# Kernel optimization log

Hardware: AMD Instinct MI355X
Metric: run time of the kernel (lower is better)

Reference implementation:

```python
import jax, jax.numpy as jnp
import numpy as np

K = 3  # n_neighbors


def setup_inputs() -> dict:
    key = jax.random.key(0)
    k1, k2, k3 = jax.random.split(key, 3)
    N, D, C, B = 400000, 27, 11, 512  # train size, 3*N_PEAKS_MAX, classes, query batch
    train_features = jax.random.normal(k1, (N, D), dtype=jnp.float32)
    label_idx = jax.random.randint(k2, (N,), 0, C)
    train_labels = jax.nn.one_hot(label_idx, C, dtype=jnp.float32)
    query = jax.random.normal(k3, (B, D), dtype=jnp.float32)
    return {"query": query, "train_features": train_features, "train_labels": train_labels}


def _divide_no_nan(x, y):
    # tf.math.divide_no_nan: 0 where denominator is 0
    y_safe = jnp.where(y != 0, y, 1.0)
    return jnp.where(y != 0, x / y_safe, 0.0)


def reference(query, train_features, train_labels):
    # scale = per-feature max abs over training set (computed in __init__)
    scale = jnp.max(jnp.abs(train_features), axis=0)            # [D]
    train_s = _divide_no_nan(train_features, scale)             # [N,D]
    q_s = _divide_no_nan(query, scale)                          # [B,D]

    xn = jnp.sum(train_s * train_s, axis=1)                     # [N]
    qn = jnp.sum(q_s * q_s, axis=1)                             # [B]
    d2 = qn[:, None] - 2.0 * jnp.einsum('bd,nd->bn', q_s, train_s) + xn[None, :]
    dist = jnp.sqrt(jnp.maximum(d2, 0.0))                       # [B,N]

    neg_kd, idx = jax.lax.top_k(-dist, K)                       # k smallest distances
    kd = -neg_kd                                                # [B,K]

    lab = train_labels[idx]                                     # [B,K,C]
    # inverse-distance weighted vote (safe against zero distances)
    kd_safe = jnp.where(kd == 0.0, 1.0, kd)
    votes = jnp.sum(lab / kd_safe[:, :, None], axis=1)          # [B,C]
    vote_res = jax.nn.one_hot(jnp.argmax(votes, axis=1), train_labels.shape[1], dtype=jnp.float32)

    # exact-match branch: if the nearest distance is 0, return its label directly
    zero_hit = (jnp.min(kd, axis=1) == 0.0)[:, None]            # [B,1]
    result = jnp.where(zero_hit, lab[:, 0, :], vote_res)        # [B,C]
    return kd, result
```

## Files before the change

kernel.cpp:

```cpp
#include <hip/hip_runtime.h>
#include <math.h>

typedef _Float16 h8 __attribute__((ext_vector_type(8)));
typedef float    f4v __attribute__((ext_vector_type(4)));

#define N_TRAIN 400000
#define DIMS    27
#define BQ      512
#define NCLS    11
#define KNN     3
#define NB      500
#define TPB     512
#define PTS_BLK 800
#define PTS_SUP 160
#define NSUP    5
#define NPT     10
#define RAWF    4320
#define TILE_B  2048
#define NC      (NB * KNN)
#define SB      512
#define RPB     784
#define SROWS   128
#define P2T     512

__global__ __launch_bounds__(256) void k_scale(const float* __restrict__ train,
                                               unsigned* __restrict__ scale_u) {
    __shared__ float st[SROWS * DIMS];
    __shared__ float sp[243];
    int tid = threadIdx.x;
    int r0 = blockIdx.x * RPB;
    int r1 = min(r0 + RPB, N_TRAIN);
    int c  = tid % DIMS;
    int rr = tid / DIMS;
    float m = 0.f;
    for (int base = r0; base < r1; base += SROWS) {
        int cnt = min(SROWS, r1 - base);
        int tot4 = (cnt * DIMS) >> 2;
        const uint4* src4 = (const uint4*)(train + (size_t)base * DIMS);
        uint4* st4 = (uint4*)st;
        for (int i = tid; i < tot4; i += 256) st4[i] = src4[i];
        __syncthreads();
        if (tid < 243) {
            for (int r = rr; r < cnt; r += 9)
                m = fmaxf(m, fabsf(st[r * DIMS + c]));
        }
        __syncthreads();
    }
    if (tid < 243) sp[tid] = m;
    __syncthreads();
    if (tid < DIMS) {
        float v = 0.f;
#pragma unroll
        for (int g = 0; g < 9; ++g) v = fmaxf(v, sp[g * DIMS + tid]);
        atomicMax(&scale_u[tid], __float_as_uint(v));
    }
}

__global__ __launch_bounds__(TPB) void k_qprep(const float* __restrict__ query,
                                               const unsigned* __restrict__ scale_u,
                                               _Float16* __restrict__ Qhi,
                                               _Float16* __restrict__ Qlo) {
    int q = threadIdx.x;
    if (q >= BQ) return;
    const float* r = query + (size_t)q * DIMS;
#pragma unroll
    for (int d = 0; d < 32; ++d) {
        _Float16 hi = (_Float16)0.f, lo = (_Float16)0.f;
        if (d < DIMS) {
            float sc = __uint_as_float(scale_u[d]);
            float inv = (sc != 0.f) ? 1.f / sc : 0.f;
            float xs = r[d] * inv;
            hi = (_Float16)xs;
            lo = (_Float16)(xs - (float)hi);
        } else if (d == 27) {
            hi = (_Float16)1.f;
        }
        Qhi[q * 32 + d] = hi;
        Qlo[q * 32 + d] = lo;
    }
}

#define TOP2(A, GI, B0, B1, I0, I1) do { \
    bool c0_ = (A) > (B0); \
    bool c1_ = (A) > (B1); \
    B1 = c0_ ? (B0) : (c1_ ? (A) : (B1)); \
    I1 = c0_ ? (I0) : (c1_ ? (GI) : (I1)); \
    B0 = c0_ ? (A) : (B0); \
    I0 = c0_ ? (GI) : (I0); \
} while (0)

__device__ __forceinline__ void insert3(float d, int i, float* bd, int* bi) {
    if (d < bd[2] || (d == bd[2] && i < bi[2])) {
        if (d < bd[1] || (d == bd[1] && i < bi[1])) {
            bd[2] = bd[1]; bi[2] = bi[1];
            if (d < bd[0] || (d == bd[0] && i < bi[0])) {
                bd[1] = bd[0]; bi[1] = bi[0];
                bd[0] = d; bi[0] = i;
            } else { bd[1] = d; bi[1] = i; }
        } else { bd[2] = d; bi[2] = i; }
    }
}

__device__ __forceinline__ void stage16(const float* g, float* l) {
    __builtin_amdgcn_global_load_lds((const __attribute__((address_space(1))) void*)g,
                                     (__attribute__((address_space(3))) void*)l, 16, 0, 0);
}

__global__ __attribute__((amdgpu_flat_work_group_size(TPB, TPB)))
__attribute__((amdgpu_waves_per_eu(4, 4)))
void k_pass1(const float* __restrict__ train,
             const unsigned* __restrict__ scale_u,
             const _Float16* __restrict__ Qhi,
             const _Float16* __restrict__ Qlo,
             float* __restrict__ cand_d,
             int* __restrict__ cand_i) {
    __shared__ float s_inv[32];
    __shared__ __align__(16) float raw[2][RAWF];
    __shared__ __align__(16) unsigned char conv[NPT * TILE_B];

    int tid = threadIdx.x;
    if (tid < 32) {
        float sc = __uint_as_float(scale_u[tid]);
        s_inv[tid] = (sc != 0.f) ? 1.f / sc : 0.f;
    }
    int lane = tid & 63, w = tid >> 6;
    int l15 = lane & 15, quad = lane >> 4;

    h8 bhi[4], blo[4];
#pragma unroll
    for (int j = 0; j < 4; ++j) {
        int qt = w * 4 + j;
        size_t e = (size_t)(qt * 16 + l15) * 32 + quad * 8;
        bhi[j] = *(const h8*)(Qhi + e);
        blo[j] = *(const h8*)(Qlo + e);
    }

    float b0[4], b1[4];
    int   i0[4], i1[4];
#pragma unroll
    for (int j = 0; j < 4; ++j) { b0[j] = -3.4e38f; b1[j] = -3.4e38f; i0[j] = 0x7fffffff; i1[j] = 0x7fffffff; }

    int p0 = blockIdx.x * PTS_BLK;
    const float* gsup = train + (size_t)p0 * DIMS;

    {
        const float* gp = gsup; float* lp = raw[0];
        stage16(gp + tid * 4, lp + tid * 4);
        stage16(gp + 2048 + tid * 4, lp + 2048 + tid * 4);
        if (tid < 56) stage16(gp + 4096 + tid * 4, lp + 4096 + tid * 4);
    }

    for (int s = 0; s < NSUP; ++s) {
        __syncthreads();

        const float* rw = raw[s & 1];
#pragma unroll
        for (int pass = 0; pass < 2; ++pass) {
            int task = tid + pass * TPB;
            if (task < PTS_SUP * 4) {
                int p = task >> 2, gq = task & 3;
                float x[8]; float part = 0.f;
#pragma unroll
                for (int i = 0; i < 8; ++i) {
                    int d = gq * 8 + i;
                    int dc = d < DIMS ? d : (DIMS - 1);
                    float v = rw[p * DIMS + dc] * s_inv[d];
                    x[i] = v;
                    part = fmaf(v, v, part);
                }
                part += __shfl_xor(part, 1, 64);
                part += __shfl_xor(part, 2, 64);
                h8 hv, lv;
#pragma unroll
                for (int i = 0; i < 8; ++i) {
                    _Float16 h = (_Float16)x[i];
                    hv[i] = h;
                    lv[i] = (_Float16)(x[i] - (float)h);
                }
                if (gq == 3) {
                    float tt = -0.5f * part;
                    _Float16 th = (_Float16)tt;
                    hv[3] = th;
                    lv[3] = (_Float16)(tt - (float)th);
                }
                unsigned char* dstb = conv + (p >> 4) * TILE_B + gq * 256 + (p & 15) * 16;
                *(h8*)dstb = hv;
                *(h8*)(dstb + 1024) = lv;
            }
        }
        __syncthreads();

        if (s + 1 < NSUP) {
            const float* gp = gsup + (size_t)(s + 1) * RAWF;
            float* lp = raw[(s + 1) & 1];
            stage16(gp + tid * 4, lp + tid * 4);
            stage16(gp + 2048 + tid * 4, lp + 2048 + tid * 4);
            if (tid < 56) stage16(gp + 4096 + tid * 4, lp + 4096 + tid * 4);
        }

        for (int t = 0; t < NPT; ++t) {
            const unsigned char* basep = conv + t * TILE_B;
            h8 ahi = *(const h8*)(basep + lane * 16);
            h8 alo = *(const h8*)(basep + 1024 + lane * 16);
            int gbase = p0 + (s * NPT + t) * 16 + quad * 4;
#pragma unroll
            for (int j = 0; j < 4; ++j) {
                f4v acc = {0.f, 0.f, 0.f, 0.f};
                acc = __builtin_amdgcn_mfma_f32_16x16x32_f16(alo, bhi[j], acc, 0, 0, 0);
                acc = __builtin_amdgcn_mfma_f32_16x16x32_f16(ahi, blo[j], acc, 0, 0, 0);
                acc = __builtin_amdgcn_mfma_f32_16x16x32_f16(ahi, bhi[j], acc, 0, 0, 0);
#pragma unroll
                for (int r = 0; r < 4; ++r)
                    TOP2(acc[r], gbase + r, b0[j], b1[j], i0[j], i1[j]);
            }
        }
    }

    int g = blockIdx.x;
#pragma unroll
    for (int j = 0; j < 4; ++j) {
        float kk[3] = {-b0[j], -b1[j], 3.4e38f};
        int   ii[3] = {i0[j], i1[j], 0x7fffffff};
#pragma unroll
        for (int step = 16; step <= 32; step <<= 1) {
            float od[3]; int oi[3];
#pragma unroll
            for (int k = 0; k < 3; ++k) {
                od[k] = __shfl_xor(kk[k], step, 64);
                oi[k] = __shfl_xor(ii[k], step, 64);
            }
#pragma unroll
            for (int k = 0; k < 3; ++k) insert3(od[k], oi[k], kk, ii);
        }
        if (quad == 0) {
            int qq = (w * 4 + j) * 16 + l15;
            size_t off = (size_t)qq * NC + (size_t)g * KNN;
#pragma unroll
            for (int k = 0; k < KNN; ++k) { cand_d[off + k] = kk[k]; cand_i[off + k] = ii[k]; }
        }
    }
}

__device__ __forceinline__ unsigned long long shfl_xor_u64(unsigned long long v, int m) {
    unsigned lo = (unsigned)v, hi = (unsigned)(v >> 32);
    lo = __shfl_xor(lo, m, 64);
    hi = __shfl_xor(hi, m, 64);
    return ((unsigned long long)hi << 32) | lo;
}

#define U64MAX 0xFFFFFFFFFFFFFFFFULL
#define CE(a, b) do { unsigned long long lo_ = (a) < (b) ? (a) : (b); \
                      unsigned long long hi_ = (a) < (b) ? (b) : (a); \
                      (a) = lo_; (b) = hi_; } while (0)

__global__ __launch_bounds__(P2T) void k_pass2(const float* __restrict__ cand_d,
                                               const int* __restrict__ cand_i,
                                               const float* __restrict__ train,
                                               const float* __restrict__ query,
                                               const unsigned* __restrict__ scale_u,
                                               const float* __restrict__ labels,
                                               float* __restrict__ out) {
    __shared__ unsigned long long smerge[64];
    int q = blockIdx.x;
    int tid = threadIdx.x, lane = tid & 63, w = tid >> 6;
    const float* cd = cand_d + (size_t)q * NC;
    const int*   ci = cand_i + (size_t)q * NC;

    unsigned long long c0 = U64MAX, c1 = U64MAX, c2 = U64MAX;
    {
        unsigned db0 = __float_as_uint(cd[tid]);
        db0 = (db0 & 0x80000000u) ? ~db0 : (db0 | 0x80000000u);
        c0 = ((unsigned long long)db0 << 32) | (unsigned)ci[tid];
        unsigned db1 = __float_as_uint(cd[tid + P2T]);
        db1 = (db1 & 0x80000000u) ? ~db1 : (db1 | 0x80000000u);
        c1 = ((unsigned long long)db1 << 32) | (unsigned)ci[tid + P2T];
        if (tid + 2 * P2T < NC) {
            unsigned db2 = __float_as_uint(cd[tid + 2 * P2T]);
            db2 = (db2 & 0x80000000u) ? ~db2 : (db2 | 0x80000000u);
            c2 = ((unsigned long long)db2 << 32) | (unsigned)ci[tid + 2 * P2T];
        }
        CE(c0, c1); CE(c0, c2); CE(c1, c2);
    }

#pragma unroll
    for (int k = 0; k < 8; ++k) {
        unsigned long long m = c0;
#pragma unroll
        for (int st = 1; st < 64; st <<= 1) {
            unsigned long long o = shfl_xor_u64(m, st);
            if (o < m) m = o;
        }
        if (lane == 0) smerge[w * 8 + k] = m;
        bool win = (c0 == m);
        c0 = win ? c1 : c0;
        c1 = win ? c2 : c1;
        c2 = win ? U64MAX : c2;
    }
    __syncthreads();
    if (w != 0) return;

    int myi = 0x7fffffff;
    {
        unsigned long long cur = smerge[lane];
#pragma unroll
        for (int k = 0; k < 8; ++k) {
            unsigned long long m = cur;
#pragma unroll
            for (int st = 1; st < 64; st <<= 1) {
                unsigned long long o = shfl_xor_u64(m, st);
                if (o < m) m = o;
            }
            if (lane == k) myi = (int)(unsigned)m;
            if (cur == m) cur = U64MAX;
        }
    }

    float inv[DIMS], qs_[DIMS], qn_ = 0.f;
#pragma unroll
    for (int d = 0; d < DIMS; ++d) {
        float sc = __uint_as_float(scale_u[d]);
        float iv = (sc != 0.f) ? 1.f / sc : 0.f;
        float v = query[(size_t)q * DIMS + d] * iv;
        inv[d] = iv; qs_[d] = v;
        qn_ = fmaf(v, v, qn_);
    }

    float myd2 = 3.4e38f;
    if (lane < 8) {
        const float* r = train + (size_t)myi * DIMS;
        float xnv = 0.f, dot = 0.f;
#pragma unroll
        for (int d = 0; d < DIMS; ++d) {
            float v = r[d] * inv[d];
            xnv = fmaf(v, v, xnv);
            dot = fmaf(qs_[d], v, dot);
        }
        myd2 = fmaf(-2.f, dot, qn_ + xnv);
    }

    float bd[KNN] = {3.4e38f, 3.4e38f, 3.4e38f};
    int   bi[KNN] = {0x7fffffff, 0x7fffffff, 0x7fffffff};
#pragma unroll
    for (int k = 0; k < 8; ++k) {
        float dk = __shfl(myd2, k, 64);
        int   ik = __shfl(myi, k, 64);
        insert3(dk, ik, bd, bi);
    }

    if (lane == 0) {
        float kd[KNN];
#pragma unroll
        for (int k = 0; k < KNN; ++k) kd[k] = sqrtf(fmaxf(bd[k], 0.f));
        float lab[KNN][NCLS];
#pragma unroll
        for (int k = 0; k < KNN; ++k) {
            const float* lr = labels + (size_t)bi[k] * NCLS;
#pragma unroll
            for (int c = 0; c < NCLS; ++c) lab[k][c] = lr[c];
        }
        float votes[NCLS];
#pragma unroll
        for (int c = 0; c < NCLS; ++c) votes[c] = 0.f;
#pragma unroll
        for (int k = 0; k < KNN; ++k) {
            float ks = (kd[k] == 0.f) ? 1.f : kd[k];
#pragma unroll
            for (int c = 0; c < NCLS; ++c) votes[c] += lab[k][c] / ks;
        }
        int best = 0; float bv = votes[0];
#pragma unroll
        for (int c = 1; c < NCLS; ++c) { if (votes[c] > bv) { bv = votes[c]; best = c; } }
        bool zero_hit = (kd[0] == 0.f);
#pragma unroll
        for (int k = 0; k < KNN; ++k) out[(size_t)q * KNN + k] = kd[k];
        float* ro = out + (size_t)BQ * KNN + (size_t)q * NCLS;
#pragma unroll
        for (int c = 0; c < NCLS; ++c)
            ro[c] = zero_hit ? lab[0][c] : ((c == best) ? 1.f : 0.f);
    }
}

extern "C" void kernel_launch(void* const* d_in, const int* in_sizes, int n_in,
                              void* d_out, int out_size, void* d_ws, size_t ws_size,
                              hipStream_t stream) {
    const float* query  = (const float*)d_in[0];
    const float* train  = (const float*)d_in[1];
    const float* labels = (const float*)d_in[2];
    float* out = (float*)d_out;

    char* ws = (char*)d_ws;
    unsigned*  scale_u = (unsigned*)ws;
    _Float16*  Qhi = (_Float16*)(ws + 128);
    _Float16*  Qlo = (_Float16*)(ws + 32896);
    float*     cand_d = (float*)(ws + 65664);
    int*       cand_i = (int*)(ws + 3137664);

    hipMemsetAsync(ws, 0, 128, stream);
    k_scale<<<SB, 256, 0, stream>>>(train, scale_u);
    k_qprep<<<1, TPB, 0, stream>>>(query, scale_u, Qhi, Qlo);
    k_pass1<<<NB, TPB, 0, stream>>>(train, scale_u, Qhi, Qlo, cand_d, cand_i);
    k_pass2<<<BQ, P2T, 0, stream>>>(cand_d, cand_i, train, query, scale_u, labels, out);
}
```

Measured before the change: 194.1 us.

## Pack score and tile index into u32 keys for per-row top-2 in pass1

```diff
diff --git a/kernel.cpp b/kernel.cpp
--- a/kernel.cpp
+++ b/kernel.cpp
@@ -22,6 +22,8 @@
 #define RPB     784
 #define SROWS   128
 #define P2T     512
+
+#define U64MAX 0xFFFFFFFFFFFFFFFFULL
 
 __global__ __launch_bounds__(256) void k_scale(const float* __restrict__ train,
                                                unsigned* __restrict__ scale_u) {
@@ -80,15 +82,6 @@
     }
 }
 
-#define TOP2(A, GI, B0, B1, I0, I1) do { \
-    bool c0_ = (A) > (B0); \
-    bool c1_ = (A) > (B1); \
-    B1 = c0_ ? (B0) : (c1_ ? (A) : (B1)); \
-    I1 = c0_ ? (I0) : (c1_ ? (GI) : (I1)); \
-    B0 = c0_ ? (A) : (B0); \
-    I0 = c0_ ? (GI) : (I0); \
-} while (0)
-
 __device__ __forceinline__ void insert3(float d, int i, float* bd, int* bi) {
     if (d < bd[2] || (d == bd[2] && i < bi[2])) {
         if (d < bd[1] || (d == bd[1] && i < bi[1])) {
@@ -101,6 +94,26 @@
     }
 }
 
+__device__ __forceinline__ unsigned long long shfl_xor_u64(unsigned long long v, int m) {
+    unsigned lo = (unsigned)v, hi = (unsigned)(v >> 32);
+    lo = __shfl_xor(lo, m, 64);
+    hi = __shfl_xor(hi, m, 64);
+    return ((unsigned long long)hi << 32) | lo;
+}
+
+__device__ __forceinline__ void ins3u64(unsigned long long e,
+                                        unsigned long long& t0,
+                                        unsigned long long& t1,
+                                        unsigned long long& t2) {
+    unsigned long long a  = e < t2 ? e : t2;
+    unsigned long long n2 = t1 > a ? t1 : a;
+    unsigned long long n1 = t1 < a ? t1 : a;
+    t2 = n2;
+    unsigned long long m1 = t0 > n1 ? t0 : n1;
+    t0 = t0 < n1 ? t0 : n1;
+    t1 = m1;
+}
+
 __device__ __forceinline__ void stage16(const float* g, float* l) {
     __builtin_amdgcn_global_load_lds((const __attribute__((address_space(1))) void*)g,
                                      (__attribute__((address_space(3))) void*)l, 16, 0, 0);
@@ -112,8 +125,7 @@
              const unsigned* __restrict__ scale_u,
              const _Float16* __restrict__ Qhi,
              const _Float16* __restrict__ Qlo,
-             float* __restrict__ cand_d,
-             int* __restrict__ cand_i) {
+             unsigned long long* __restrict__ cand) {
     __shared__ float s_inv[32];
     __shared__ __align__(16) float raw[2][RAWF];
     __shared__ __align__(16) unsigned char conv[NPT * TILE_B];
@@ -135,10 +147,11 @@
         blo[j] = *(const h8*)(Qlo + e);
     }
 
-    float b0[4], b1[4];
-    int   i0[4], i1[4];
-#pragma unroll
-    for (int j = 0; j < 4; ++j) { b0[j] = -3.4e38f; b1[j] = -3.4e38f; i0[j] = 0x7fffffff; i1[j] = 0x7fffffff; }
+    unsigned kb0[4][4], kb1[4][4];
+#pragma unroll
+    for (int j = 0; j < 4; ++j)
+#pragma unroll
+        for (int r = 0; r < 4; ++r) { kb0[j][r] = 0u; kb1[j][r] = 0u; }
 
     int p0 = blockIdx.x * PTS_BLK;
     const float* gsup = train + (size_t)p0 * DIMS;
@@ -202,59 +215,64 @@
             const unsigned char* basep = conv + t * TILE_B;
             h8 ahi = *(const h8*)(basep + lane * 16);
             h8 alo = *(const h8*)(basep + 1024 + lane * 16);
-            int gbase = p0 + (s * NPT + t) * 16 + quad * 4;
+            unsigned ic = 63u - (unsigned)(s * NPT + t);
 #pragma unroll
             for (int j = 0; j < 4; ++j) {
-                f4v acc = {0.f, 0.f, 0.f, 0.f};
+                f4v acc = {64.f, 64.f, 64.f, 64.f};
                 acc = __builtin_amdgcn_mfma_f32_16x16x32_f16(alo, bhi[j], acc, 0, 0, 0);
                 acc = __builtin_amdgcn_mfma_f32_16x16x32_f16(ahi, blo[j], acc, 0, 0, 0);
                 acc = __builtin_amdgcn_mfma_f32_16x16x32_f16(ahi, bhi[j], acc, 0, 0, 0);
 #pragma unroll
-                for (int r = 0; r < 4; ++r)
-                    TOP2(acc[r], gbase + r, b0[j], b1[j], i0[j], i1[j]);
+                for (int r = 0; r < 4; ++r) {
+                    unsigned key = (__float_as_uint(acc[r]) & 0xFFFFFFC0u) | ic;
+                    unsigned b0 = kb0[j][r];
+                    unsigned m  = key < b0 ? key : b0;
+                    kb0[j][r]   = key > b0 ? key : b0;
+                    unsigned b1 = kb1[j][r];
+                    kb1[j][r]   = m > b1 ? m : b1;
+                }
             }
         }
     }
 
     int g = blockIdx.x;
+    int qr4 = quad * 4;
 #pragma unroll
     for (int j = 0; j < 4; ++j) {
-        float kk[3] = {-b0[j], -b1[j], 3.4e38f};
-        int   ii[3] = {i0[j], i1[j], 0x7fffffff};
+        unsigned long long t0 = U64MAX, t1 = U64MAX, t2 = U64MAX;
+#pragma unroll
+        for (int r = 0; r < 4; ++r) {
+#pragma unroll
+            for (int h = 0; h < 2; ++h) {
+                unsigned k = h ? kb1[j][r] : kb0[j][r];
+                unsigned tile = 63u - (k & 63u);
+                unsigned gi = (unsigned)(p0 + (int)tile * 16 + qr4 + r);
+                unsigned long long e = ((unsigned long long)(~(k | 63u)) << 32) | gi;
+                ins3u64(e, t0, t1, t2);
+            }
+        }
 #pragma unroll
         for (int step = 16; step <= 32; step <<= 1) {
-            float od[3]; int oi[3];
-#pragma unroll
-            for (int k = 0; k < 3; ++k) {
-                od[k] = __shfl_xor(kk[k], step, 64);
-                oi[k] = __shfl_xor(ii[k], step, 64);
-            }
-#pragma unroll
-            for (int k = 0; k < 3; ++k) insert3(od[k], oi[k], kk, ii);
+            unsigned long long o0 = shfl_xor_u64(t0, step);
+            unsigned long long o1 = shfl_xor_u64(t1, step);
+            unsigned long long o2 = shfl_xor_u64(t2, step);
+            ins3u64(o0, t0, t1, t2);
+            ins3u64(o1, t0, t1, t2);
+            ins3u64(o2, t0, t1, t2);
         }
         if (quad == 0) {
             int qq = (w * 4 + j) * 16 + l15;
             size_t off = (size_t)qq * NC + (size_t)g * KNN;
-#pragma unroll
-            for (int k = 0; k < KNN; ++k) { cand_d[off + k] = kk[k]; cand_i[off + k] = ii[k]; }
-        }
-    }
-}
-
-__device__ __forceinline__ unsigned long long shfl_xor_u64(unsigned long long v, int m) {
-    unsigned lo = (unsigned)v, hi = (unsigned)(v >> 32);
-    lo = __shfl_xor(lo, m, 64);
-    hi = __shfl_xor(hi, m, 64);
-    return ((unsigned long long)hi << 32) | lo;
-}
-
-#define U64MAX 0xFFFFFFFFFFFFFFFFULL
+            cand[off + 0] = t0; cand[off + 1] = t1; cand[off + 2] = t2;
+        }
+    }
+}
+
 #define CE(a, b) do { unsigned long long lo_ = (a) < (b) ? (a) : (b); \
                       unsigned long long hi_ = (a) < (b) ? (b) : (a); \
                       (a) = lo_; (b) = hi_; } while (0)
 
-__global__ __launch_bounds__(P2T) void k_pass2(const float* __restrict__ cand_d,
-                                               const int* __restrict__ cand_i,
+__global__ __launch_bounds__(P2T) void k_pass2(const unsigned long long* __restrict__ cand,
                                                const float* __restrict__ train,
                                                const float* __restrict__ query,
                                                const unsigned* __restrict__ scale_u,
@@ -263,24 +281,12 @@
     __shared__ unsigned long long smerge[64];
     int q = blockIdx.x;
     int tid = threadIdx.x, lane = tid & 63, w = tid >> 6;
-    const float* cd = cand_d + (size_t)q * NC;
-    const int*   ci = cand_i + (size_t)q * NC;
-
-    unsigned long long c0 = U64MAX, c1 = U64MAX, c2 = U64MAX;
-    {
-        unsigned db0 = __float_as_uint(cd[tid]);
-        db0 = (db0 & 0x80000000u) ? ~db0 : (db0 | 0x80000000u);
-        c0 = ((unsigned long long)db0 << 32) | (unsigned)ci[tid];
-        unsigned db1 = __float_as_uint(cd[tid + P2T]);
-        db1 = (db1 & 0x80000000u) ? ~db1 : (db1 | 0x80000000u);
-        c1 = ((unsigned long long)db1 << 32) | (unsigned)ci[tid + P2T];
-        if (tid + 2 * P2T < NC) {
-            unsigned db2 = __float_as_uint(cd[tid + 2 * P2T]);
-            db2 = (db2 & 0x80000000u) ? ~db2 : (db2 | 0x80000000u);
-            c2 = ((unsigned long long)db2 << 32) | (unsigned)ci[tid + 2 * P2T];
-        }
-        CE(c0, c1); CE(c0, c2); CE(c1, c2);
-    }
+    const unsigned long long* cd = cand + (size_t)q * NC;
+
+    unsigned long long c0 = cd[tid];
+    unsigned long long c1 = cd[tid + P2T];
+    unsigned long long c2 = (tid + 2 * P2T < NC) ? cd[tid + 2 * P2T] : U64MAX;
+    CE(c0, c1); CE(c0, c2); CE(c1, c2);
 
 #pragma unroll
     for (int k = 0; k < 8; ++k) {
@@ -392,12 +398,11 @@
     unsigned*  scale_u = (unsigned*)ws;
     _Float16*  Qhi = (_Float16*)(ws + 128);
     _Float16*  Qlo = (_Float16*)(ws + 32896);
-    float*     cand_d = (float*)(ws + 65664);
-    int*       cand_i = (int*)(ws + 3137664);
+    unsigned long long* cand = (unsigned long long*)(ws + 65664);
 
     hipMemsetAsync(ws, 0, 128, stream);
     k_scale<<<SB, 256, 0, stream>>>(train, scale_u);
     k_qprep<<<1, TPB, 0, stream>>>(query, scale_u, Qhi, Qlo);
-    k_pass1<<<NB, TPB, 0, stream>>>(train, scale_u, Qhi, Qlo, cand_d, cand_i);
-    k_pass2<<<BQ, P2T, 0, stream>>>(cand_d, cand_i, train, query, scale_u, labels, out);
-}
+    k_pass1<<<NB, TPB, 0, stream>>>(train, scale_u, Qhi, Qlo, cand);
+    k_pass2<<<BQ, P2T, 0, stream>>>(cand, train, query, scale_u, labels, out);
+}
```

After: 188.6 us. -2.9%, faster.
